# Optimization experiments

Measured on AMD Instinct MI355X. Metric: run time of the kernel, lower is better.

## Reference

```python
import jax, jax.numpy as jnp
import numpy as np
import math

EPS = 1e-5
HEADS = 8

def _lin(x, w, b):
    return x @ w.T + b

def _ln(x, g, b):
    m = x.mean(-1, keepdims=True)
    v = ((x - m) ** 2).mean(-1, keepdims=True)
    return (x - m) / jnp.sqrt(v + EPS) * g + b

def _bn_eval(x, g, b):
    # BatchNorm1d eval with init running stats (mean=0, var=1)
    return x / jnp.sqrt(1.0 + EPS) * g[None, :, None] + b[None, :, None]

def _conv1d(x, w, b, pad):
    y = jax.lax.conv_general_dilated(x, w, (1,), [(pad, pad)],
                                     dimension_numbers=('NCH', 'OIH', 'NCH'))
    return y + b[None, :, None]

def _interp_linear(x, out_len):
    # F.interpolate(mode='linear', align_corners=False) on last axis
    L = x.shape[-1]
    src = (jnp.arange(out_len) + 0.5) * (L / out_len) - 0.5
    src = jnp.clip(src, 0.0, L - 1)
    i0 = jnp.floor(src).astype(jnp.int32)
    i1 = jnp.minimum(i0 + 1, L - 1)
    w = (src - i0).astype(x.dtype)
    return x[..., i0] * (1.0 - w) + x[..., i1] * w

def setup_inputs():
    key = jax.random.key(0)
    ks = iter(jax.random.split(key, 64))
    def nrm(shape, scale=0.02):
        return jax.random.normal(next(ks), shape, dtype=jnp.float32) * scale
    B, T, N, H, HOR, C = 2, 64, 2048, 128, 24, 32
    return dict(
        x=jax.random.normal(next(ks), (B, T, N), dtype=jnp.float32),
        tc_w=nrm((C, 1, 3), 0.2), tc_b=jnp.zeros((C,)), tc_bn_g=jnp.ones((C,)), tc_bn_b=jnp.zeros((C,)),
        fp_w=nrm((H, C * T)), fp_b=jnp.zeros((H,)), fp_ln_g=jnp.ones((H,)), fp_ln_b=jnp.zeros((H,)),
        q_w=nrm((H, H)), q_b=jnp.zeros((H,)),
        k_w=nrm((H, H)), k_b=jnp.zeros((H,)),
        v_w=nrm((H, H)), v_b=jnp.zeros((H,)),
        o_w=nrm((H, H)), o_b=jnp.zeros((H,)),
        adj=nrm((1, HEADS, N, N), 0.02),
        s0_w=nrm((H, H, 1), 0.05), s0_b=jnp.zeros((H,)), s0_bn_g=jnp.ones((H,)), s0_bn_b=jnp.zeros((H,)),
        s1_w=nrm((H, H, 2), 0.05), s1_b=jnp.zeros((H,)), s1_bn_g=jnp.ones((H,)), s1_bn_b=jnp.zeros((H,)),
        fusion_weight=jnp.ones((2,)),
        fu_w=nrm((H, H)), fu_b=jnp.zeros((H,)), fu_ln_g=jnp.ones((H,)), fu_ln_b=jnp.zeros((H,)),
        pr1_w=nrm((H, H)), pr1_b=jnp.zeros((H,)), pr_ln_g=jnp.ones((H,)), pr_ln_b=jnp.zeros((H,)),
        pr2_w=nrm((HOR, H)), pr2_b=jnp.zeros((HOR,)),
        rg_w=nrm((HOR, H)), rg_b=jnp.zeros((HOR,)),
    )

def _forward(x, tc_w, tc_b, tc_bn_g, tc_bn_b, fp_w, fp_b, fp_ln_g, fp_ln_b,
             q_w, q_b, k_w, k_b, v_w, v_b, o_w, o_b, adj,
             s0_w, s0_b, s0_bn_g, s0_bn_b, s1_w, s1_b, s1_bn_g, s1_bn_b,
             fusion_weight, fu_w, fu_b, fu_ln_g, fu_ln_b,
             pr1_w, pr1_b, pr_ln_g, pr_ln_b, pr2_w, pr2_b, rg_w, rg_b):
    B, T, N = x.shape
    H = q_w.shape[0]
    hd = H // HEADS
    x_last = x[:, -1, :]                                  # (B, N)
    # temporal conv over the window per node
    xt = x.transpose(0, 2, 1).reshape(B * N, 1, T)
    f = jax.nn.relu(_bn_eval(_conv1d(xt, tc_w, tc_b, 1), tc_bn_g, tc_bn_b))
    f = f.reshape(B, N, -1)                               # (B, N, 32*T)
    feats = jax.nn.relu(_ln(_lin(f, fp_w, fp_b), fp_ln_g, fp_ln_b))
    # adaptive graph attention with learnable adjacency bias
    q = _lin(feats, q_w, q_b).reshape(B, N, HEADS, hd)
    k = _lin(feats, k_w, k_b).reshape(B, N, HEADS, hd)
    v = _lin(feats, v_w, v_b).reshape(B, N, HEADS, hd)
    scores = jnp.einsum('bnhd,bmhd->bhnm', q, k) / math.sqrt(hd) + adj
    attn = jax.nn.softmax(scores, axis=-1)                # (B, HEADS, N, N)
    reg = jnp.float32(1e-4) * jnp.mean(jnp.abs(attn))
    go = jnp.einsum('bhnm,bmhd->bnhd', attn, v).reshape(B, N, H)
    gf = _lin(go, o_w, o_b)                               # (B, N, H)
    # multi-scale fusion (conv over node axis, kernels 1 and 2)
    xc = gf.transpose(0, 2, 1)                            # (B, H, N)
    f0 = jax.nn.relu(_bn_eval(_conv1d(xc, s0_w, s0_b, 0), s0_bn_g, s0_bn_b))
    f1 = jax.nn.relu(_bn_eval(_conv1d(xc, s1_w, s1_b, 1), s1_bn_g, s1_bn_b))  # (B,H,N+1)
    f1 = _interp_linear(f1, N)
    alpha = jax.nn.softmax(fusion_weight)
    fused = (alpha[0] * f0 + alpha[1] * f1).transpose(0, 2, 1)
    ff = jax.nn.relu(_ln(_lin(fused, fu_w, fu_b), fu_ln_g, fu_ln_b))
    # progressive prediction refinement
    h = jax.nn.relu(_ln(_lin(ff, pr1_w, pr1_b), pr_ln_g, pr_ln_b))
    preds = _lin(h, pr2_w, pr2_b)                         # (B, N, horizon)
    gates = jax.nn.sigmoid(_lin(ff, rg_w, rg_b))
    refined = gates * x_last[..., None] + (1.0 - gates) * preds
    return refined.transpose(0, 2, 1), reg                # (B, horizon, N), scalar

def reference(x, tc_w, tc_b, tc_bn_g, tc_bn_b, fp_w, fp_b, fp_ln_g, fp_ln_b,
              q_w, q_b, k_w, k_b, v_w, v_b, o_w, o_b, adj,
              s0_w, s0_b, s0_bn_g, s0_bn_b, s1_w, s1_b, s1_bn_g, s1_bn_b,
              fusion_weight, fu_w, fu_b, fu_ln_g, fu_ln_b,
              pr1_w, pr1_b, pr_ln_g, pr_ln_b, pr2_w, pr2_b, rg_w, rg_b):
    return _forward(x, tc_w, tc_b, tc_bn_g, tc_bn_b, fp_w, fp_b, fp_ln_g, fp_ln_b,
                    q_w, q_b, k_w, k_b, v_w, v_b, o_w, o_b, adj,
                    s0_w, s0_b, s0_bn_g, s0_bn_b, s1_w, s1_b, s1_bn_g, s1_bn_b,
                    fusion_weight, fu_w, fu_b, fu_ln_g, fu_ln_b,
                    pr1_w, pr1_b, pr_ln_g, pr_ln_b, pr2_w, pr2_b, rg_w, rg_b)
```

## Files before the change

kernel.cpp:

```cpp
#include <hip/hip_runtime.h>

using f32x4  = __attribute__((ext_vector_type(4))) float;
using bf16x8 = __attribute__((ext_vector_type(8))) short;

#define DEV static __device__ __forceinline__

DEV unsigned short f2bf(float f){
  unsigned u = __float_as_uint(f);
  unsigned r = (u + 0x7FFFu + ((u >> 16) & 1u)) >> 16;
  return (unsigned short)r;
}

DEV int vperm(int n){
  return (n & ~63) | (n & 32) | ((n & 0xC) << 1) | ((n & 0x10) >> 2) | (n & 3);
}

__global__ __launch_bounds__(256) void prep_kernel(
    const float* __restrict__ fp_w, const float* __restrict__ q_w,
    const float* __restrict__ k_w, const float* __restrict__ v_w,
    const float* __restrict__ o_w, const float* __restrict__ s0_w,
    const float* __restrict__ s1_w, const float* __restrict__ fu_w,
    const float* __restrict__ pr1_w, const float* __restrict__ pr2_w,
    const float* __restrict__ rg_w,
    unsigned short* __restrict__ fpw_bf, unsigned short* __restrict__ wcat_bf,
    float* __restrict__ o_wT, float* __restrict__ fu_wT, float* __restrict__ pr1_wT,
    float* __restrict__ s0_wT, float* __restrict__ s1_wT0, float* __restrict__ s1_wT1,
    float* __restrict__ pr2_wT, float* __restrict__ rg_wT){
  int i = blockIdx.x * 256 + threadIdx.x;
  const int stride = 128 * 256;
  for (int idx = i; idx < 128 * 2048; idx += stride) fpw_bf[idx] = f2bf(fp_w[idx]);
  for (int idx = i; idx < 384 * 128; idx += stride){
    int c = idx >> 7, k = idx & 127;
    float v;
    if (c < 128)      v = q_w[c * 128 + k] * 0.25f;
    else if (c < 256) v = k_w[(c - 128) * 128 + k];
    else              v = v_w[(c - 256) * 128 + k];
    wcat_bf[idx] = f2bf(v);
  }
  for (int idx = i; idx < 128 * 128; idx += stride){
    int k = idx >> 7, c = idx & 127;
    o_wT[idx]   = o_w[c * 128 + k];
    fu_wT[idx]  = fu_w[c * 128 + k];
    pr1_wT[idx] = pr1_w[c * 128 + k];
    s0_wT[idx]  = s0_w[c * 128 + k];
    s1_wT0[idx] = s1_w[(c * 128 + k) * 2 + 0];
    s1_wT1[idx] = s1_w[(c * 128 + k) * 2 + 1];
  }
  for (int idx = i; idx < 128 * 24; idx += stride){
    int k = idx / 24, c = idx % 24;
    pr2_wT[idx] = pr2_w[c * 128 + k];
    rg_wT[idx]  = rg_w[c * 128 + k];
  }
}

__global__ __launch_bounds__(512) void convfeatqkv_kernel(
    const float* __restrict__ x, const float* __restrict__ tc_w,
    const float* __restrict__ tc_b, const float* __restrict__ bn_g,
    const float* __restrict__ bn_b,
    const unsigned short* __restrict__ fpw, const float* __restrict__ fp_b,
    const float* __restrict__ ln_g, const float* __restrict__ ln_b,
    const unsigned short* __restrict__ wcat, const float* __restrict__ q_b,
    const float* __restrict__ k_b, const float* __restrict__ v_b,
    unsigned short* __restrict__ qo, unsigned short* __restrict__ ko,
    unsigned short* __restrict__ vTp){
  __shared__ float xs[64][17];
  __shared__ unsigned short fs[16 * 1024];
  __shared__ float pre[16][128];
  __shared__ unsigned short ft[16 * 128];
  __shared__ float stat[16][2];
  int t = threadIdx.x;
  int lane = t & 63, w = t >> 6;
  int l15 = lane & 15, g = lane >> 4;
  int row0 = blockIdx.x * 16;
  int b = row0 >> 11, n0 = row0 & 2047;
  const float bninv = rsqrtf(1.0f + 1e-5f);
  for (int e = t; e < 1024; e += 512){
    int tt = e >> 4, nn2 = e & 15;
    xs[tt][nn2] = x[(size_t)(b * 64 + tt) * 2048 + n0 + nn2];
  }
  __syncthreads();
  int nn = t & 15, chl = (t >> 4) & 15, th = t >> 8;
  int c0 = w * 16;
  f32x4 acc = {0.f,0.f,0.f,0.f};
  const unsigned short* bp = fpw + (size_t)(c0 + l15) * 2048 + g * 8;
  const char* fsbase = (const char*)fs + l15 * 2048;
  int aswz = (l15 & 7) << 4;
  char* fsrow = (char*)fs + nn * 2048;
  int wswz = (nn & 7) << 4;
  for (int half = 0; half < 2; half++){
    {
      int ch = half * 16 + chl;
      float cw0 = tc_w[ch * 3 + 0], cw1 = tc_w[ch * 3 + 1], cw2 = tc_w[ch * 3 + 2];
      float cb = tc_b[ch];
      float csc = bninv * bn_g[ch], cbb = bn_b[ch];
      int t0 = th * 32;
      float xprev = (t0 > 0) ? xs[t0 - 1][nn] : 0.f;
      float xcur  = xs[t0][nn];
      #pragma unroll
      for (int j = 0; j < 4; j++){
        bf16x8 pack;
        #pragma unroll
        for (int i2 = 0; i2 < 8; i2++){
          int tt = t0 + j * 8 + i2;
          float xnext = (tt < 63) ? xs[tt + 1][nn] : 0.f;
          float y = (xprev * cw0 + xcur * cw1 + xnext * cw2 + cb) * csc + cbb;
          pack[i2] = (short)f2bf(fmaxf(y, 0.f));
          xprev = xcur; xcur = xnext;
        }
        int kl = chl * 64 + t0 + j * 8;
        *(bf16x8*)(fsrow + ((kl * 2) ^ wswz)) = pack;
      }
    }
    __syncthreads();
    #pragma unroll 4
    for (int kk = 0; kk < 1024; kk += 32){
      bf16x8 a  = *(const bf16x8*)(fsbase + (((kk + g * 8) * 2) ^ aswz));
      bf16x8 b0 = *(const bf16x8*)(bp + half * 1024 + kk);
      acc = __builtin_amdgcn_mfma_f32_16x16x32_bf16(a, b0, acc, 0, 0, 0);
    }
    __syncthreads();
  }
  #pragma unroll
  for (int r = 0; r < 4; r++)
    pre[g * 4 + r][c0 + l15] = acc[r] + fp_b[c0 + l15];
  __syncthreads();
  if (t < 256){
    int r = t >> 4, j = t & 15;
    float s = 0.f, ss = 0.f;
    #pragma unroll
    for (int q = 0; q < 8; q++){ float v = pre[r][j + q * 16]; s += v; ss += v * v; }
    #pragma unroll
    for (int m = 1; m < 16; m <<= 1){ s += __shfl_xor(s, m, 64); ss += __shfl_xor(ss, m, 64); }
    if (j == 0){
      float mean = s * (1.f / 128.f);
      stat[r][0] = mean;
      stat[r][1] = rsqrtf(ss * (1.f / 128.f) - mean * mean + 1e-5f);
    }
  }
  __syncthreads();
  if (t < 256){
    int r = t >> 4, j = t & 15;
    float mean = stat[r][0], rstd = stat[r][1];
    bf16x8 outv;
    #pragma unroll
    for (int q = 0; q < 8; q++){
      int cc = j * 8 + q;
      float v = (pre[r][cc] - mean) * rstd * ln_g[cc] + ln_b[cc];
      outv[q] = (short)f2bf(fmaxf(v, 0.f));
    }
    int byte = r * 256 + ((j * 16) ^ ((r & 7) << 4));
    *(bf16x8*)((char*)ft + byte) = outv;
  }
  __syncthreads();
  f32x4 acc3[3] = {{0,0,0,0},{0,0,0,0},{0,0,0,0}};
  #pragma unroll
  for (int kk = 0; kk < 128; kk += 32){
    int abyte = l15 * 256 + (((kk + g * 8) * 2) ^ ((l15 & 7) << 4));
    bf16x8 a = *(const bf16x8*)((const char*)ft + abyte);
    #pragma unroll
    for (int ci = 0; ci < 3; ci++){
      int cc0 = w * 48 + ci * 16;
      bf16x8 bb = *(const bf16x8*)(wcat + (size_t)(cc0 + l15) * 128 + g * 8 + kk);
      acc3[ci] = __builtin_amdgcn_mfma_f32_16x16x32_bf16(a, bb, acc3[ci], 0, 0, 0);
    }
  }
  #pragma unroll
  for (int ci = 0; ci < 3; ci++){
    int c = w * 48 + ci * 16 + l15;
    int mat = c >> 7, cm = c & 127;
    int hh = cm >> 4, d = cm & 15;
    float bias = (mat == 0) ? q_b[cm] * 0.25f : (mat == 1 ? k_b[cm] : v_b[cm]);
    int bh = b * 8 + hh;
    #pragma unroll
    for (int r = 0; r < 4; r++){
      int n = n0 + g * 4 + r;
      unsigned short bv = f2bf(acc3[ci][r] + bias);
      if (mat == 0)      qo[((size_t)bh * 2048 + n) * 16 + d] = bv;
      else if (mat == 1) ko[((size_t)bh * 2048 + n) * 16 + d] = bv;
      else               vTp[((size_t)bh * 16 + d) * 2048 + vperm(n)] = bv;
    }
  }
}

__global__ __launch_bounds__(512) void attn_kernel(
    const unsigned short* __restrict__ qo, const unsigned short* __restrict__ ko,
    const unsigned short* __restrict__ vTp, const float* __restrict__ adj,
    float* __restrict__ go){
  __shared__ float red_acc[8][2][16][16];
  __shared__ float red_rs[8][2][16];
  int t = threadIdx.x, lane = t & 63, w = t >> 6;
  int l15 = lane & 15, g = lane >> 4;
  int h = blockIdx.x >> 7;
  int row0 = (blockIdx.x & 127) * 16;
  const bf16x8 zf = {0,0,0,0,0,0,0,0};
  const f32x4 z4 = {0.f,0.f,0.f,0.f};
  bf16x8 qf[2];
  #pragma unroll
  for (int b2 = 0; b2 < 2; b2++){
    if (g < 2) qf[b2] = *(const bf16x8*)(qo + ((size_t)(b2 * 8 + h) * 2048 + row0 + l15) * 16 + g * 8);
    else       qf[b2] = zf;
  }
  f32x4 accv[2] = {{0.f,0.f,0.f,0.f},{0.f,0.f,0.f,0.f}};
  float rsp[2] = {0.f, 0.f};
  const float* adjrow = adj + ((size_t)h * 2048 + row0 + l15) * 2048 + g * 4;
  const int mbeg = w * 256;
  for (int m0 = mbeg; m0 < mbeg + 256; m0 += 64){
    f32x4 adjv[4];
    #pragma unroll
    for (int s = 0; s < 4; s++)
      adjv[s] = *(const f32x4*)(adjrow + m0 + s * 16);
    #pragma unroll
    for (int b2 = 0; b2 < 2; b2++){
      int bh = b2 * 8 + h;
      const unsigned short* kbase = ko + (size_t)bh * 2048 * 16;
      f32x4 sf[4];
      #pragma unroll
      for (int s = 0; s < 4; s++){
        bf16x8 kf;
        if (g < 2) kf = *(const bf16x8*)(kbase + (size_t)(m0 + s * 16 + l15) * 16 + g * 8);
        else       kf = zf;
        sf[s] = __builtin_amdgcn_mfma_f32_16x16x32_bf16(kf, qf[b2], z4, 0, 0, 0);
      }
      bf16x8 pf[2];
      float partial = 0.f;
      #pragma unroll
      for (int s = 0; s < 4; s++){
        #pragma unroll
        for (int r = 0; r < 4; r++){
          float p = __expf(sf[s][r] + adjv[s][r]);
          partial += p;
          pf[s >> 1][(s & 1) * 4 + r] = (short)f2bf(p);
        }
      }
      rsp[b2] += partial;
      const unsigned short* vbase = vTp + ((size_t)bh * 16 + l15) * 2048 + m0;
      bf16x8 vf0 = *(const bf16x8*)(vbase + g * 8);
      bf16x8 vf1 = *(const bf16x8*)(vbase + 32 + g * 8);
      accv[b2] = __builtin_amdgcn_mfma_f32_16x16x32_bf16(vf0, pf[0], accv[b2], 0, 0, 0);
      accv[b2] = __builtin_amdgcn_mfma_f32_16x16x32_bf16(vf1, pf[1], accv[b2], 0, 0, 0);
    }
  }
  #pragma unroll
  for (int b2 = 0; b2 < 2; b2++){
    float s = rsp[b2];
    s += __shfl_xor(s, 16, 64);
    s += __shfl_xor(s, 32, 64);
    #pragma unroll
    for (int r = 0; r < 4; r++) red_acc[w][b2][g * 4 + r][l15] = accv[b2][r];
    if (lane < 16) red_rs[w][b2][l15] = s;
  }
  __syncthreads();
  {
    int b2 = t >> 8, qq = (t >> 4) & 15, d = t & 15;
    float v = 0.f, den = 0.f;
    #pragma unroll
    for (int ww = 0; ww < 8; ww++){ v += red_acc[ww][b2][d][qq]; den += red_rs[ww][b2][qq]; }
    go[((size_t)b2 * 2048 + row0 + qq) * 128 + h * 16 + d] = v / den;
  }
}

__global__ __launch_bounds__(512) void tail_kernel(
    const float* __restrict__ go, const float* __restrict__ x,
    const float* __restrict__ o_wT, const float* __restrict__ o_b,
    const float* __restrict__ s0_wT, const float* __restrict__ s0_b,
    const float* __restrict__ s0_g, const float* __restrict__ s0_bb,
    const float* __restrict__ s1_wT0, const float* __restrict__ s1_wT1,
    const float* __restrict__ s1_b, const float* __restrict__ s1_g,
    const float* __restrict__ s1_bb, const float* __restrict__ fw,
    const float* __restrict__ fu_wT, const float* __restrict__ fu_b,
    const float* __restrict__ fu_g, const float* __restrict__ fu_bb,
    const float* __restrict__ pr1_wT, const float* __restrict__ pr1_b,
    const float* __restrict__ pr_g, const float* __restrict__ pr_bb,
    const float* __restrict__ pr2_wT, const float* __restrict__ pr2_b,
    const float* __restrict__ rg_wT, const float* __restrict__ rg_b,
    float* __restrict__ out){
  __shared__ float go_s[20][128];
  __shared__ float gf_s[21][128];
  __shared__ float f1_s[17][128];
  __shared__ float fu_in[16][128];
  __shared__ float pre_s[16][128];
  __shared__ float ff_s[16][128];
  __shared__ float h_s[16][128];
  __shared__ float stat[16][2];
  int t = threadIdx.x;
  int b = blockIdx.x >> 7;
  int n0 = (blockIdx.x & 127) * 16;
  for (int e = t; e < 20 * 128; e += 512){
    int lr = e >> 7, cc = e & 127;
    int gn = n0 - 1 + lr;
    go_s[lr][cc] = (lr < 18 && gn >= 0 && gn < 2048) ? go[((size_t)b * 2048 + gn) * 128 + cc] : 0.f;
  }
  __syncthreads();
  int c = t & 127, q4 = t >> 7;
  const float bninv = rsqrtf(1.0f + 1e-5f);
  {
    float acc[5];
    float bias = o_b[c];
    #pragma unroll
    for (int i = 0; i < 5; i++) acc[i] = bias;
    for (int k = 0; k < 128; k++){
      float wv = o_wT[k * 128 + c];
      #pragma unroll
      for (int i = 0; i < 5; i++) acc[i] += go_s[i * 4 + q4][k] * wv;
    }
    #pragma unroll
    for (int i = 0; i < 5; i++){
      int lr = i * 4 + q4;
      int gn = n0 - 1 + lr;
      gf_s[lr][c] = (lr < 18 && gn >= 0 && gn < 2048) ? acc[i] : 0.f;
    }
    if (t < 128) gf_s[20][t] = 0.f;
  }
  __syncthreads();
  {
    float acc[5];
    float bias = s1_b[c];
    #pragma unroll
    for (int i = 0; i < 5; i++) acc[i] = bias;
    for (int k = 0; k < 128; k++){
      float w0 = s1_wT0[k * 128 + c], w1 = s1_wT1[k * 128 + c];
      #pragma unroll
      for (int i = 0; i < 5; i++)
        acc[i] += gf_s[i * 4 + q4][k] * w0 + gf_s[i * 4 + q4 + 1][k] * w1;
    }
    float sc = s1_g[c] * bninv, bb2 = s1_bb[c];
    #pragma unroll
    for (int i = 0; i < 5; i++){
      int lr = i * 4 + q4;
      if (lr < 17) f1_s[lr][c] = fmaxf(acc[i] * sc + bb2, 0.f);
    }
  }
  __syncthreads();
  {
    float acc[4];
    float bias = s0_b[c];
    #pragma unroll
    for (int i = 0; i < 4; i++) acc[i] = bias;
    for (int k = 0; k < 128; k++){
      float wv = s0_wT[k * 128 + c];
      #pragma unroll
      for (int i = 0; i < 4; i++) acc[i] += gf_s[i * 4 + q4 + 1][k] * wv;
    }
    float e0 = __expf(fw[0]), e1 = __expf(fw[1]);
    float a0 = e0 / (e0 + e1), a1 = e1 / (e0 + e1);
    float sc = s0_g[c] * bninv, bb2 = s0_bb[c];
    #pragma unroll
    for (int i = 0; i < 4; i++){
      int lr = i * 4 + q4;
      int n = n0 + lr;
      float f0 = fmaxf(acc[i] * sc + bb2, 0.f);
      float wn = (n + 0.5f) * (1.0f / 2048.0f);
      fu_in[lr][c] = a0 * f0 + a1 * ((1.f - wn) * f1_s[lr][c] + wn * f1_s[lr + 1][c]);
    }
  }
  __syncthreads();
  {
    float acc[4];
    float bias = fu_b[c];
    #pragma unroll
    for (int i = 0; i < 4; i++) acc[i] = bias;
    for (int k = 0; k < 128; k++){
      float wv = fu_wT[k * 128 + c];
      #pragma unroll
      for (int i = 0; i < 4; i++) acc[i] += fu_in[i * 4 + q4][k] * wv;
    }
    #pragma unroll
    for (int i = 0; i < 4; i++) pre_s[i * 4 + q4][c] = acc[i];
  }
  __syncthreads();
  if (t < 256){
    int r = t >> 4, j = t & 15;
    float s = 0.f, ss = 0.f;
    #pragma unroll
    for (int q = 0; q < 8; q++){ float v = pre_s[r][j + q * 16]; s += v; ss += v * v; }
    #pragma unroll
    for (int m = 1; m < 16; m <<= 1){ s += __shfl_xor(s, m, 64); ss += __shfl_xor(ss, m, 64); }
    if (j == 0){ float mean = s * (1.f / 128.f); stat[r][0] = mean;
                 stat[r][1] = rsqrtf(ss * (1.f / 128.f) - mean * mean + 1e-5f); }
  }
  __syncthreads();
  if (t < 256){
    int r = t >> 4, j = t & 15;
    float mean = stat[r][0], rstd = stat[r][1];
    #pragma unroll
    for (int q = 0; q < 8; q++){
      int cc = j * 8 + q;
      ff_s[r][cc] = fmaxf((pre_s[r][cc] - mean) * rstd * fu_g[cc] + fu_bb[cc], 0.f);
    }
  }
  __syncthreads();
  {
    float acc[4];
    float bias = pr1_b[c];
    #pragma unroll
    for (int i = 0; i < 4; i++) acc[i] = bias;
    for (int k = 0; k < 128; k++){
      float wv = pr1_wT[k * 128 + c];
      #pragma unroll
      for (int i = 0; i < 4; i++) acc[i] += ff_s[i * 4 + q4][k] * wv;
    }
    #pragma unroll
    for (int i = 0; i < 4; i++) pre_s[i * 4 + q4][c] = acc[i];
  }
  __syncthreads();
  if (t < 256){
    int r = t >> 4, j = t & 15;
    float s = 0.f, ss = 0.f;
    #pragma unroll
    for (int q = 0; q < 8; q++){ float v = pre_s[r][j + q * 16]; s += v; ss += v * v; }
    #pragma unroll
    for (int m = 1; m < 16; m <<= 1){ s += __shfl_xor(s, m, 64); ss += __shfl_xor(ss, m, 64); }
    if (j == 0){ float mean = s * (1.f / 128.f); stat[r][0] = mean;
                 stat[r][1] = rsqrtf(ss * (1.f / 128.f) - mean * mean + 1e-5f); }
  }
  __syncthreads();
  if (t < 256){
    int r = t >> 4, j = t & 15;
    float mean = stat[r][0], rstd = stat[r][1];
    #pragma unroll
    for (int q = 0; q < 8; q++){
      int cc = j * 8 + q;
      h_s[r][cc] = fmaxf((pre_s[r][cc] - mean) * rstd * pr_g[cc] + pr_bb[cc], 0.f);
    }
  }
  __syncthreads();
  if (t < 384){
    int lr = t / 24, cc = t % 24;
    float accp = pr2_b[cc], accg = rg_b[cc];
    for (int k = 0; k < 128; k++){
      accp += h_s[lr][k] * pr2_wT[k * 24 + cc];
      accg += ff_s[lr][k] * rg_wT[k * 24 + cc];
    }
    float gate = 1.f / (1.f + __expf(-accg));
    int n = n0 + lr;
    float xl = x[((size_t)b * 64 + 63) * 2048 + n];
    out[((size_t)b * 24 + cc) * 2048 + n] = gate * xl + (1.f - gate) * accp;
  }
  if (blockIdx.x == 0 && t == 0) out[2 * 24 * 2048] = 1e-4f / 2048.0f;
}

extern "C" void kernel_launch(void* const* d_in, const int* in_sizes, int n_in,
                              void* d_out, int out_size, void* d_ws, size_t ws_size,
                              hipStream_t stream){
  const float* x       = (const float*)d_in[0];
  const float* tc_w    = (const float*)d_in[1];
  const float* tc_b    = (const float*)d_in[2];
  const float* tc_bn_g = (const float*)d_in[3];
  const float* tc_bn_b = (const float*)d_in[4];
  const float* fp_w    = (const float*)d_in[5];
  const float* fp_b    = (const float*)d_in[6];
  const float* fp_ln_g = (const float*)d_in[7];
  const float* fp_ln_b = (const float*)d_in[8];
  const float* q_w     = (const float*)d_in[9];
  const float* q_b     = (const float*)d_in[10];
  const float* k_w     = (const float*)d_in[11];
  const float* k_b     = (const float*)d_in[12];
  const float* v_w     = (const float*)d_in[13];
  const float* v_b     = (const float*)d_in[14];
  const float* o_w     = (const float*)d_in[15];
  const float* o_b     = (const float*)d_in[16];
  const float* adj     = (const float*)d_in[17];
  const float* s0_w    = (const float*)d_in[18];
  const float* s0_b    = (const float*)d_in[19];
  const float* s0_bn_g = (const float*)d_in[20];
  const float* s0_bn_b = (const float*)d_in[21];
  const float* s1_w    = (const float*)d_in[22];
  const float* s1_b    = (const float*)d_in[23];
  const float* s1_bn_g = (const float*)d_in[24];
  const float* s1_bn_b = (const float*)d_in[25];
  const float* fusion_w= (const float*)d_in[26];
  const float* fu_w    = (const float*)d_in[27];
  const float* fu_b    = (const float*)d_in[28];
  const float* fu_ln_g = (const float*)d_in[29];
  const float* fu_ln_b = (const float*)d_in[30];
  const float* pr1_w   = (const float*)d_in[31];
  const float* pr1_b   = (const float*)d_in[32];
  const float* pr_ln_g = (const float*)d_in[33];
  const float* pr_ln_b = (const float*)d_in[34];
  const float* pr2_w   = (const float*)d_in[35];
  const float* pr2_b   = (const float*)d_in[36];
  const float* rg_w    = (const float*)d_in[37];
  const float* rg_b    = (const float*)d_in[38];
  float* out = (float*)d_out;

  char* ws = (char*)d_ws;
  size_t off = 0;
  auto alloc = [&](size_t bytes) -> void* {
    void* p = ws + off;
    off += (bytes + 255) & ~(size_t)255;
    return p;
  };
  unsigned short* fpw_bf  = (unsigned short*)alloc((size_t)128 * 2048 * 2);
  unsigned short* wcat_bf = (unsigned short*)alloc((size_t)384 * 128 * 2);
  unsigned short* q_bf    = (unsigned short*)alloc((size_t)16 * 2048 * 16 * 2);
  unsigned short* k_bf    = (unsigned short*)alloc((size_t)16 * 2048 * 16 * 2);
  unsigned short* vTp_bf  = (unsigned short*)alloc((size_t)16 * 2048 * 16 * 2);
  float* go     = (float*)alloc((size_t)4096 * 128 * 4);
  float* o_wT   = (float*)alloc(128 * 128 * 4);
  float* fu_wT  = (float*)alloc(128 * 128 * 4);
  float* pr1_wT = (float*)alloc(128 * 128 * 4);
  float* s0_wT  = (float*)alloc(128 * 128 * 4);
  float* s1_wT0 = (float*)alloc(128 * 128 * 4);
  float* s1_wT1 = (float*)alloc(128 * 128 * 4);
  float* pr2_wT = (float*)alloc(128 * 24 * 4);
  float* rg_wT  = (float*)alloc(128 * 24 * 4);
  if (off > ws_size) return;

  prep_kernel<<<128, 256, 0, stream>>>(fp_w, q_w, k_w, v_w, o_w, s0_w, s1_w,
                                       fu_w, pr1_w, pr2_w, rg_w, fpw_bf, wcat_bf,
                                       o_wT, fu_wT, pr1_wT, s0_wT, s1_wT0, s1_wT1,
                                       pr2_wT, rg_wT);
  convfeatqkv_kernel<<<256, 512, 0, stream>>>(x, tc_w, tc_b, tc_bn_g, tc_bn_b,
                                              fpw_bf, fp_b, fp_ln_g, fp_ln_b,
                                              wcat_bf, q_b, k_b, v_b,
                                              q_bf, k_bf, vTp_bf);
  attn_kernel<<<1024, 512, 0, stream>>>(q_bf, k_bf, vTp_bf, adj, go);
  tail_kernel<<<256, 512, 0, stream>>>(go, x, o_wT, o_b, s0_wT, s0_b, s0_bn_g, s0_bn_b,
                                       s1_wT0, s1_wT1, s1_b, s1_bn_g, s1_bn_b, fusion_w,
                                       fu_wT, fu_b, fu_ln_g, fu_ln_b, pr1_wT, pr1_b,
                                       pr_ln_g, pr_ln_b, pr2_wT, pr2_b, rg_wT, rg_b, out);
}
```

Measured before the change: 124.1 us.

## Split MFMA accumulators, prefetch adj nontemporally, halve tail tile rows

The feature GEMM now alternates between two independent MFMA accumulators, which shortens the dependency chain. The attention kernel double-buffers the adj row loads with nontemporal loads, so the next 64-column chunk is fetched during the current chunk's compute. The tail kernel processes 8 nodes per block instead of 16 and launches 512 blocks, giving more parallelism and less halo padding. The cost is reloading the tail weights in twice as many blocks, and higher register pressure in attention.

```diff
diff --git a/kernel.cpp b/kernel.cpp
--- a/kernel.cpp
+++ b/kernel.cpp
@@ -81,7 +81,7 @@
   __syncthreads();
   int nn = t & 15, chl = (t >> 4) & 15, th = t >> 8;
   int c0 = w * 16;
-  f32x4 acc = {0.f,0.f,0.f,0.f};
+  f32x4 accA = {0.f,0.f,0.f,0.f}, accB = {0.f,0.f,0.f,0.f};
   const unsigned short* bp = fpw + (size_t)(c0 + l15) * 2048 + g * 8;
   const char* fsbase = (const char*)fs + l15 * 2048;
   int aswz = (l15 & 7) << 4;
@@ -112,17 +112,20 @@
       }
     }
     __syncthreads();
-    #pragma unroll 4
-    for (int kk = 0; kk < 1024; kk += 32){
-      bf16x8 a  = *(const bf16x8*)(fsbase + (((kk + g * 8) * 2) ^ aswz));
+    #pragma unroll 2
+    for (int kk = 0; kk < 1024; kk += 64){
+      bf16x8 a0 = *(const bf16x8*)(fsbase + (((kk + g * 8) * 2) ^ aswz));
       bf16x8 b0 = *(const bf16x8*)(bp + half * 1024 + kk);
-      acc = __builtin_amdgcn_mfma_f32_16x16x32_bf16(a, b0, acc, 0, 0, 0);
+      accA = __builtin_amdgcn_mfma_f32_16x16x32_bf16(a0, b0, accA, 0, 0, 0);
+      bf16x8 a1 = *(const bf16x8*)(fsbase + (((kk + 32 + g * 8) * 2) ^ aswz));
+      bf16x8 b1 = *(const bf16x8*)(bp + half * 1024 + kk + 32);
+      accB = __builtin_amdgcn_mfma_f32_16x16x32_bf16(a1, b1, accB, 0, 0, 0);
     }
     __syncthreads();
   }
   #pragma unroll
   for (int r = 0; r < 4; r++)
-    pre[g * 4 + r][c0 + l15] = acc[r] + fp_b[c0 + l15];
+    pre[g * 4 + r][c0 + l15] = accA[r] + accB[r] + fp_b[c0 + l15];
   __syncthreads();
   if (t < 256){
     int r = t >> 4, j = t & 15;
@@ -204,11 +207,17 @@
   float rsp[2] = {0.f, 0.f};
   const float* adjrow = adj + ((size_t)h * 2048 + row0 + l15) * 2048 + g * 4;
   const int mbeg = w * 256;
+  f32x4 adjc[4], adjn[4];
+  #pragma unroll
+  for (int s = 0; s < 4; s++)
+    adjc[s] = __builtin_nontemporal_load((const f32x4*)(adjrow + mbeg + s * 16));
   for (int m0 = mbeg; m0 < mbeg + 256; m0 += 64){
-    f32x4 adjv[4];
-    #pragma unroll
-    for (int s = 0; s < 4; s++)
-      adjv[s] = *(const f32x4*)(adjrow + m0 + s * 16);
+    bool more = (m0 + 64) < (mbeg + 256);
+    if (more){
+      #pragma unroll
+      for (int s = 0; s < 4; s++)
+        adjn[s] = __builtin_nontemporal_load((const f32x4*)(adjrow + m0 + 64 + s * 16));
+    }
     #pragma unroll
     for (int b2 = 0; b2 < 2; b2++){
       int bh = b2 * 8 + h;
@@ -227,7 +236,7 @@
       for (int s = 0; s < 4; s++){
         #pragma unroll
         for (int r = 0; r < 4; r++){
-          float p = __expf(sf[s][r] + adjv[s][r]);
+          float p = __expf(sf[s][r] + adjc[s][r]);
           partial += p;
           pf[s >> 1][(s & 1) * 4 + r] = (short)f2bf(p);
         }
@@ -238,6 +247,10 @@
       bf16x8 vf1 = *(const bf16x8*)(vbase + 32 + g * 8);
       accv[b2] = __builtin_amdgcn_mfma_f32_16x16x32_bf16(vf0, pf[0], accv[b2], 0, 0, 0);
       accv[b2] = __builtin_amdgcn_mfma_f32_16x16x32_bf16(vf1, pf[1], accv[b2], 0, 0, 0);
+    }
+    if (more){
+      #pragma unroll
+      for (int s = 0; s < 4; s++) adjc[s] = adjn[s];
     }
   }
   #pragma unroll
@@ -274,101 +287,89 @@
     const float* __restrict__ pr2_wT, const float* __restrict__ pr2_b,
     const float* __restrict__ rg_wT, const float* __restrict__ rg_b,
     float* __restrict__ out){
-  __shared__ float go_s[20][128];
-  __shared__ float gf_s[21][128];
-  __shared__ float f1_s[17][128];
-  __shared__ float fu_in[16][128];
-  __shared__ float pre_s[16][128];
-  __shared__ float ff_s[16][128];
-  __shared__ float h_s[16][128];
-  __shared__ float stat[16][2];
+  __shared__ float go_s[10][128];
+  __shared__ float gf_s[10][128];
+  __shared__ float f1_s[9][128];
+  __shared__ float fu_in[8][128];
+  __shared__ float pre_s[8][128];
+  __shared__ float ff_s[8][128];
+  __shared__ float h_s[8][128];
+  __shared__ float stat[8][2];
   int t = threadIdx.x;
-  int b = blockIdx.x >> 7;
-  int n0 = (blockIdx.x & 127) * 16;
-  for (int e = t; e < 20 * 128; e += 512){
+  int b = blockIdx.x >> 8;
+  int n0 = (blockIdx.x & 255) * 8;
+  for (int e = t; e < 10 * 128; e += 512){
     int lr = e >> 7, cc = e & 127;
     int gn = n0 - 1 + lr;
-    go_s[lr][cc] = (lr < 18 && gn >= 0 && gn < 2048) ? go[((size_t)b * 2048 + gn) * 128 + cc] : 0.f;
+    go_s[lr][cc] = (gn >= 0 && gn < 2048) ? go[((size_t)b * 2048 + gn) * 128 + cc] : 0.f;
   }
   __syncthreads();
   int c = t & 127, q4 = t >> 7;
   const float bninv = rsqrtf(1.0f + 1e-5f);
   {
-    float acc[5];
     float bias = o_b[c];
-    #pragma unroll
-    for (int i = 0; i < 5; i++) acc[i] = bias;
+    float a0 = bias, a1 = bias, a2 = bias;
     for (int k = 0; k < 128; k++){
       float wv = o_wT[k * 128 + c];
-      #pragma unroll
-      for (int i = 0; i < 5; i++) acc[i] += go_s[i * 4 + q4][k] * wv;
-    }
-    #pragma unroll
-    for (int i = 0; i < 5; i++){
-      int lr = i * 4 + q4;
-      int gn = n0 - 1 + lr;
-      gf_s[lr][c] = (lr < 18 && gn >= 0 && gn < 2048) ? acc[i] : 0.f;
-    }
-    if (t < 128) gf_s[20][t] = 0.f;
+      a0 += go_s[q4][k] * wv;
+      a1 += go_s[q4 + 4][k] * wv;
+      if (q4 < 2) a2 += go_s[q4 + 8][k] * wv;
+    }
+    int gn = n0 - 1 + q4;
+    gf_s[q4][c]     = (gn >= 0 && gn < 2048) ? a0 : 0.f;
+    gf_s[q4 + 4][c] = (gn + 4 < 2048) ? a1 : 0.f;
+    if (q4 < 2) gf_s[q4 + 8][c] = (gn + 8 < 2048) ? a2 : 0.f;
   }
   __syncthreads();
   {
-    float acc[5];
     float bias = s1_b[c];
-    #pragma unroll
-    for (int i = 0; i < 5; i++) acc[i] = bias;
+    float a0 = bias, a1 = bias, a2 = bias;
     for (int k = 0; k < 128; k++){
       float w0 = s1_wT0[k * 128 + c], w1 = s1_wT1[k * 128 + c];
-      #pragma unroll
-      for (int i = 0; i < 5; i++)
-        acc[i] += gf_s[i * 4 + q4][k] * w0 + gf_s[i * 4 + q4 + 1][k] * w1;
+      a0 += gf_s[q4][k] * w0 + gf_s[q4 + 1][k] * w1;
+      a1 += gf_s[q4 + 4][k] * w0 + gf_s[q4 + 5][k] * w1;
+      if (q4 == 0) a2 += gf_s[8][k] * w0 + gf_s[9][k] * w1;
     }
     float sc = s1_g[c] * bninv, bb2 = s1_bb[c];
-    #pragma unroll
-    for (int i = 0; i < 5; i++){
-      int lr = i * 4 + q4;
-      if (lr < 17) f1_s[lr][c] = fmaxf(acc[i] * sc + bb2, 0.f);
-    }
+    f1_s[q4][c]     = fmaxf(a0 * sc + bb2, 0.f);
+    f1_s[q4 + 4][c] = fmaxf(a1 * sc + bb2, 0.f);
+    if (q4 == 0) f1_s[8][c] = fmaxf(a2 * sc + bb2, 0.f);
   }
   __syncthreads();
   {
-    float acc[4];
     float bias = s0_b[c];
-    #pragma unroll
-    for (int i = 0; i < 4; i++) acc[i] = bias;
+    float a0 = bias, a1 = bias;
     for (int k = 0; k < 128; k++){
       float wv = s0_wT[k * 128 + c];
-      #pragma unroll
-      for (int i = 0; i < 4; i++) acc[i] += gf_s[i * 4 + q4 + 1][k] * wv;
+      a0 += gf_s[q4 + 1][k] * wv;
+      a1 += gf_s[q4 + 5][k] * wv;
     }
     float e0 = __expf(fw[0]), e1 = __expf(fw[1]);
-    float a0 = e0 / (e0 + e1), a1 = e1 / (e0 + e1);
+    float al0 = e0 / (e0 + e1), al1 = e1 / (e0 + e1);
     float sc = s0_g[c] * bninv, bb2 = s0_bb[c];
     #pragma unroll
-    for (int i = 0; i < 4; i++){
-      int lr = i * 4 + q4;
+    for (int i2 = 0; i2 < 2; i2++){
+      int lr = q4 + i2 * 4;
+      float f0 = fmaxf((i2 ? a1 : a0) * sc + bb2, 0.f);
       int n = n0 + lr;
-      float f0 = fmaxf(acc[i] * sc + bb2, 0.f);
       float wn = (n + 0.5f) * (1.0f / 2048.0f);
-      fu_in[lr][c] = a0 * f0 + a1 * ((1.f - wn) * f1_s[lr][c] + wn * f1_s[lr + 1][c]);
+      fu_in[lr][c] = al0 * f0 + al1 * ((1.f - wn) * f1_s[lr][c] + wn * f1_s[lr + 1][c]);
     }
   }
   __syncthreads();
   {
-    float acc[4];
     float bias = fu_b[c];
-    #pragma unroll
-    for (int i = 0; i < 4; i++) acc[i] = bias;
+    float a0 = bias, a1 = bias;
     for (int k = 0; k < 128; k++){
       float wv = fu_wT[k * 128 + c];
-      #pragma unroll
-      for (int i = 0; i < 4; i++) acc[i] += fu_in[i * 4 + q4][k] * wv;
-    }
-    #pragma unroll
-    for (int i = 0; i < 4; i++) pre_s[i * 4 + q4][c] = acc[i];
-  }
-  __syncthreads();
-  if (t < 256){
+      a0 += fu_in[q4][k] * wv;
+      a1 += fu_in[q4 + 4][k] * wv;
+    }
+    pre_s[q4][c] = a0;
+    pre_s[q4 + 4][c] = a1;
+  }
+  __syncthreads();
+  if (t < 128){
     int r = t >> 4, j = t & 15;
     float s = 0.f, ss = 0.f;
     #pragma unroll
@@ -379,7 +380,7 @@
                  stat[r][1] = rsqrtf(ss * (1.f / 128.f) - mean * mean + 1e-5f); }
   }
   __syncthreads();
-  if (t < 256){
+  if (t < 128){
     int r = t >> 4, j = t & 15;
     float mean = stat[r][0], rstd = stat[r][1];
     #pragma unroll
@@ -390,20 +391,18 @@
   }
   __syncthreads();
   {
-    float acc[4];
     float bias = pr1_b[c];
-    #pragma unroll
-    for (int i = 0; i < 4; i++) acc[i] = bias;
+    float a0 = bias, a1 = bias;
     for (int k = 0; k < 128; k++){
       float wv = pr1_wT[k * 128 + c];
-      #pragma unroll
-      for (int i = 0; i < 4; i++) acc[i] += ff_s[i * 4 + q4][k] * wv;
-    }
-    #pragma unroll
-    for (int i = 0; i < 4; i++) pre_s[i * 4 + q4][c] = acc[i];
-  }
-  __syncthreads();
-  if (t < 256){
+      a0 += ff_s[q4][k] * wv;
+      a1 += ff_s[q4 + 4][k] * wv;
+    }
+    pre_s[q4][c] = a0;
+    pre_s[q4 + 4][c] = a1;
+  }
+  __syncthreads();
+  if (t < 128){
     int r = t >> 4, j = t & 15;
     float s = 0.f, ss = 0.f;
     #pragma unroll
@@ -414,7 +413,7 @@
                  stat[r][1] = rsqrtf(ss * (1.f / 128.f) - mean * mean + 1e-5f); }
   }
   __syncthreads();
-  if (t < 256){
+  if (t < 128){
     int r = t >> 4, j = t & 15;
     float mean = stat[r][0], rstd = stat[r][1];
     #pragma unroll
@@ -424,7 +423,7 @@
     }
   }
   __syncthreads();
-  if (t < 384){
+  if (t < 192){
     int lr = t / 24, cc = t % 24;
     float accp = pr2_b[cc], accg = rg_b[cc];
     for (int k = 0; k < 128; k++){
@@ -515,7 +514,7 @@
                                               wcat_bf, q_b, k_b, v_b,
                                               q_bf, k_bf, vTp_bf);
   attn_kernel<<<1024, 512, 0, stream>>>(q_bf, k_bf, vTp_bf, adj, go);
-  tail_kernel<<<256, 512, 0, stream>>>(go, x, o_wT, o_b, s0_wT, s0_b, s0_bn_g, s0_bn_b,
+  tail_kernel<<<512, 512, 0, stream>>>(go, x, o_wT, o_b, s0_wT, s0_b, s0_bn_g, s0_bn_b,
                                        s1_wT0, s1_wT1, s1_b, s1_bn_g, s1_bn_b, fusion_w,
                                        fu_wT, fu_b, fu_ln_g, fu_ln_b, pr1_wT, pr1_b,
                                        pr_ln_g, pr_ln_b, pr2_wT, pr2_b, rg_wT, rg_b, out);
```

New measurement: 152.1 us. +22.6%, slower.
